# Kernel optimization log

Hardware: AMD Instinct MI355X
Metric: run time of the kernel (lower is better)

The kernel has to match this reference:

```python
import jax, jax.numpy as jnp
import numpy as np

D_MODEL, D_STATE, EXPAND = 1024, 128, 2
E = D_MODEL * EXPAND          # 2048
N = D_STATE                   # 128
H = 1
P = E
TD = D_STATE // 2             # 64
Z_DIM = E + E + N + N + H + H + TD + H  # 4369
EPS = 1e-05
B_SZ, L = 4, 2048


def setup_inputs() -> dict:
    key = jax.random.key(0)
    ks = jax.random.split(key, 6)
    u = jax.random.normal(ks[0], (B_SZ, L, D_MODEL), dtype=jnp.float32)
    W_in = jax.random.normal(ks[1], (Z_DIM, D_MODEL), dtype=jnp.float32) * 0.02
    W_out = jax.random.normal(ks[2], (D_MODEL, E), dtype=jnp.float32) * 0.02
    w_normB = jnp.ones((N,), jnp.float32)
    w_normC = jnp.ones((N,), jnp.float32)
    B_bias = jnp.ones((N,), jnp.float32)
    C_bias = jnp.ones((N,), jnp.float32)
    # dt_bias buffer: dt_i ~ logU(0.001, 0.1); dt_bias = dt_i + log(-expm1(-dt_i))
    dt_i = jnp.exp(jax.random.uniform(ks[3], (H,)) * (np.log(0.1) - np.log(0.001)) + np.log(0.001))
    dt_i = jnp.clip(dt_i, 1e-4, None)
    dt_bias = dt_i + jnp.log(-jnp.expm1(-dt_i))
    A_log = jnp.full((H,), np.log(0.5), jnp.float32)
    return {"u": u, "W_in": W_in, "w_normB": w_normB, "w_normC": w_normC,
            "B_bias": B_bias, "C_bias": C_bias, "dt_bias": dt_bias,
            "A_log": A_log, "W_out": W_out}


def _rms(x, w):
    return x * jax.lax.rsqrt(jnp.mean(x * x, axis=-1, keepdims=True) + EPS) * w


def _rope(x, ang):
    half = x.shape[-1] // 2
    x1, x2 = x[..., :half], x[..., half:]
    c, s = jnp.cos(ang), jnp.sin(ang)
    return jnp.concatenate([x1 * c - x2 * s, x1 * s + x2 * c], axis=-1)


def reference(u, W_in, w_normB, w_normC, B_bias, C_bias, dt_bias, A_log, W_out):
    Bb, Ls, _ = u.shape
    z = u @ W_in.T  # [B, L, Z_DIM]
    o = 0
    def take(n):
        nonlocal o
        r = z[..., o:o + n]; o += n; return r
    x = jax.nn.silu(take(E))
    gate = jax.nn.silu(take(E))
    B_ = take(N)
    C_ = take(N)
    dt_ = take(H)
    A_ = take(H)
    th = take(TD)
    lam_ = take(H)

    dt = jax.nn.softplus(dt_ + dt_bias)          # [B, L, H]
    A = -jax.nn.softplus(A_ + A_log)             # [B, L, H]
    lam = jax.nn.sigmoid(lam_)                   # [B, L, H]
    alpha = jnp.exp(dt * A)                      # [B, L, H]

    B_ = _rms(B_, w_normB) + B_bias
    C_ = _rms(C_, w_normC) + C_bias
    ca = jnp.cumsum(jnp.mean(dt, axis=-1, keepdims=True) * th, axis=1)  # [B, L, TD]
    B_ = _rope(B_, ca)
    C_ = _rope(C_, ca)

    xh = x.reshape(Bb, Ls, H, P)
    xp = jnp.concatenate([jnp.zeros_like(xh[:, :1]), xh[:, :-1]], axis=1)  # roll + zero t=0
    lh = lam[..., None]
    xt = lh * xh + (1.0 - lh) * alpha[..., None] * xp  # [B, L, H, P]

    # fallback SSM: per-channel mean drive, per-head scalar A (mean over batch+time)
    u_mean = jnp.mean(xt, axis=-1)               # [B, L, H]
    A_bar = jnp.mean(A, axis=(0, 1))             # [H]
    dA = jnp.exp(dt * A_bar)                     # [B, L, H]
    dBu = dt[..., None] * B_[:, :, None, :] * u_mean[..., None]  # [B, L, H, N]

    def step(state, xs):
        dA_t, dBu_t, C_t = xs                    # [B,H], [B,H,N], [B,N]
        state = dA_t[..., None] * state + dBu_t  # [B, H, N]
        y_t = jnp.einsum('bhn,bn->bh', state, C_t)
        return state, y_t

    state0 = jnp.zeros((Bb, H, N), dtype=xt.dtype)
    _, ys = jax.lax.scan(step, state0,
                         (jnp.moveaxis(dA, 1, 0), jnp.moveaxis(dBu, 1, 0), jnp.moveaxis(C_, 1, 0)))
    outs = jnp.moveaxis(ys, 0, 1)                # [B, L, H]
    y = jnp.broadcast_to(outs, (Bb, Ls, E))      # H=1 expanded to E
    return (y * gate) @ W_out.T
```

## Files before the change

### kernel.cpp

```cpp
#include <hip/hip_runtime.h>
#include <cstdint>
#include <cstddef>

typedef __bf16 bf16_t;
typedef bf16_t bf16x8 __attribute__((ext_vector_type(8)));
typedef float f32x4 __attribute__((ext_vector_type(4)));

#define B_SZ    4
#define LSEQ    2048
#define DMODEL  1024
#define EDIM    2048
#define ZDIM    4419
#define ZPAD    4608
#define ROWS    (B_SZ*LSEQ)
#define EPSV    1e-5f

#define SCHUNK  128
#define SCLEN   (LSEQ/SCHUNK)
#define RCH     128
#define RCLEN   (LSEQ/RCH)

__device__ __forceinline__ float softplus_f(float x){
  return fmaxf(x, 0.f) + log1pf(expf(-fabsf(x)));
}
__device__ __forceinline__ float sigmoid_f(float x){ return 1.f/(1.f+expf(-x)); }
__device__ __forceinline__ float silu_f(float x){ return x/(1.f+expf(-x)); }

__device__ __forceinline__ void gload_lds16(const void* g, void* l){
  __builtin_amdgcn_global_load_lds(
      (const __attribute__((address_space(1))) void*)g,
      (__attribute__((address_space(3))) void*)l, 16, 0, 0);
}

__device__ __forceinline__ float blockReduce128(float v, float* red, int t){
  red[t] = v; __syncthreads();
  #pragma unroll
  for (int off = 64; off > 0; off >>= 1){
    if (t < off) red[t] += red[t+off];
    __syncthreads();
  }
  float r = red[0];
  __syncthreads();
  return r;
}

__global__ __launch_bounds__(256) void prep_kernel(
    const float* __restrict__ u, const float* __restrict__ win, const float* __restrict__ wout,
    bf16_t* __restrict__ ubf, bf16_t* __restrict__ winbf, bf16_t* __restrict__ woutbf,
    float* __restrict__ Asum, float* __restrict__ xraw)
{
  size_t i = (size_t)blockIdx.x*256 + threadIdx.x;
  if (i == 0) Asum[0] = 0.f;
  if (i < ROWS) xraw[i] = 0.f;
  const size_t NU = (size_t)ROWS*DMODEL;
  const size_t NW = (size_t)ZPAD*DMODEL;
  const size_t NO = (size_t)DMODEL*EDIM;
  if (i < NU){ ubf[i] = (bf16_t)u[i]; return; }
  i -= NU;
  if (i < NW){
    size_t n = i >> 10;
    winbf[i] = (n < (size_t)ZDIM) ? (bf16_t)win[i] : (bf16_t)0.f;
    return;
  }
  i -= NW;
  if (i < NO) woutbf[i] = (bf16_t)wout[i];
}

template<int BM, int KDIM, int NXT, int MODE>
__global__ __launch_bounds__(512, 2) void gemmDP_kernel(
    const bf16_t* __restrict__ A, const bf16_t* __restrict__ W,
    float* __restrict__ xraw, bf16_t* __restrict__ o_g, float* __restrict__ o_z,
    const float* __restrict__ scale, float* __restrict__ o_f)
{
  constexpr int BN = 256;
  constexpr int NT = KDIM/64;
  constexpr int MR = BM/32;
  constexpr int BUFE = (BM+BN)*64;
  __shared__ __align__(16) bf16_t lds[BUFE*3];

  const int tid = threadIdx.x;
  const int wid = tid>>6, lane = tid&63;
  const int wr = wid>>2, wc = wid&3;
  const int lr = lane&15;

  const int nwg = NXT*(ROWS/BM);
  const int id = blockIdx.x;
  const int rid = (id & 7)*(nwg>>3) + (id>>3);
  const int bx = rid % NXT, by = rid / NXT;
  const int m0 = by*BM, n0 = bx*BN;

  f32x4 acc[MR][4] = {};

  auto stage = [&](int buf, int t){
    bf16_t* lA = lds + buf*BUFE;
    bf16_t* lB = lA + BM*64;
    const int k0 = t*64;
    #pragma unroll
    for (int q = 0; q < BM/64; ++q){
      int cidx = q*512 + tid;
      int row = cidx>>3, sc = (cidx&7) ^ (row&7);
      gload_lds16(A + (size_t)(m0+row)*KDIM + k0 + sc*8,
                  lA + (size_t)(q*512 + wid*64)*8);
    }
    #pragma unroll
    for (int q = 0; q < BN/64; ++q){
      int cidx = q*512 + tid;
      int row = cidx>>3, sc = (cidx&7) ^ (row&7);
      gload_lds16(W + (size_t)(n0+row)*KDIM + k0 + sc*8,
                  lB + (size_t)(q*512 + wid*64)*8);
    }
  };

  auto compute = [&](int buf){
    const bf16_t* lA = lds + buf*BUFE;
    const bf16_t* lB = lA + BM*64;
    #pragma unroll
    for (int kk = 0; kk < 2; ++kk){
      const int g = kk*4 + (lane>>4);
      bf16x8 bfr[4], af[MR];
      #pragma unroll
      for (int n = 0; n < 4; ++n){
        int rr = wc*64 + n*16 + lr;
        bfr[n] = *(const bf16x8*)&lB[rr*64 + ((g^(rr&7))<<3)];
      }
      #pragma unroll
      for (int m = 0; m < MR; ++m){
        int rr = wr*(BM/2) + m*16 + lr;
        af[m] = *(const bf16x8*)&lA[rr*64 + ((g^(rr&7))<<3)];
      }
      __builtin_amdgcn_s_setprio(1);
      #pragma unroll
      for (int m = 0; m < MR; ++m)
        #pragma unroll
        for (int n = 0; n < 4; ++n)
          acc[m][n] = __builtin_amdgcn_mfma_f32_16x16x32_bf16(af[m], bfr[n], acc[m][n], 0,0,0);
      __builtin_amdgcn_s_setprio(0);
    }
  };

  stage(0, 0);
  stage(1, 1);
  int cur = 0;
  for (int t = 0; t + 2 < NT; ++t){
    int nb = cur + 2; if (nb >= 3) nb -= 3;
    stage(nb, t+2);
    asm volatile("s_waitcnt vmcnt(12)" ::: "memory");
    asm volatile("s_barrier" ::: "memory");
    compute(cur);
    asm volatile("s_barrier" ::: "memory");
    if (++cur == 3) cur = 0;
  }
  asm volatile("s_waitcnt vmcnt(6)" ::: "memory");
  asm volatile("s_barrier" ::: "memory");
  compute(cur);
  asm volatile("s_barrier" ::: "memory");
  if (++cur == 3) cur = 0;
  asm volatile("s_waitcnt vmcnt(0)" ::: "memory");
  asm volatile("s_barrier" ::: "memory");
  compute(cur);

  if (MODE == 0 && n0 < 2048){
    #pragma unroll
    for (int m = 0; m < MR; ++m){
      #pragma unroll
      for (int i = 0; i < 4; ++i){
        float p = 0.f;
        #pragma unroll
        for (int n = 0; n < 4; ++n) p += silu_f(acc[m][n][i]);
        #pragma unroll
        for (int off = 8; off > 0; off >>= 1) p += __shfl_xor(p, off);
        if (lr == 0){
          int r = m0 + wr*(BM/2) + m*16 + ((lane>>4)<<2) + i;
          atomicAdd(xraw + r, p);
        }
      }
    }
  } else {
    #pragma unroll
    for (int m = 0; m < MR; ++m){
      int rowb = m0 + wr*(BM/2) + m*16 + ((lane>>4)<<2);
      #pragma unroll
      for (int n = 0; n < 4; ++n){
        int col = n0 + wc*64 + n*16 + lr;
        #pragma unroll
        for (int i = 0; i < 4; ++i){
          int r = rowb + i;
          float v = acc[m][n][i];
          if (MODE == 0){
            if (col < 4096)      o_g[(size_t)r*EDIM + (col-2048)] = (bf16_t)silu_f(v);
            else if (col < 4480) o_z[(size_t)r*384 + (col-4096)]  = v;
          } else {
            o_f[(size_t)r*DMODEL + col] = v * scale[r];
          }
        }
      }
    }
  }
}

__global__ __launch_bounds__(128) void fuse_kernel(
    const float* __restrict__ xraw, const float* __restrict__ zs,
    const float* __restrict__ wnB, const float* __restrict__ wnC,
    const float* __restrict__ Bb, const float* __restrict__ Cb,
    const float* __restrict__ dtb, const float* __restrict__ Alog,
    float* __restrict__ Bn, float* __restrict__ Cn, float* __restrict__ dtth,
    float* __restrict__ dts, float* __restrict__ alphas, float* __restrict__ lams,
    float* __restrict__ xbar, float* Asum)
{
  __shared__ float red[128];
  int r = blockIdx.x, t = threadIdx.x;
  const float* zr = zs + (size_t)r*384;
  float bv = zr[t], cv = zr[128+t];
  float b2 = blockReduce128(bv*bv, red, t);
  float c2 = blockReduce128(cv*cv, red, t);
  float rb = rsqrtf(b2*(1.f/128.f) + EPSV);
  float rc = rsqrtf(c2*(1.f/128.f) + EPSV);
  Bn[(size_t)r*128 + t] = bv*rb*wnB[t] + Bb[t];
  Cn[(size_t)r*128 + t] = cv*rc*wnC[t] + Cb[t];

  float dt = softplus_f(zr[256] + dtb[0]);
  if (t < 64) dtth[(size_t)r*64 + t] = dt * zr[258+t];
  if (t == 0){
    float Av  = -softplus_f(zr[257] + Alog[0]);
    float lam = sigmoid_f(zr[322]);
    dts[r]    = dt;
    alphas[r] = expf(dt*Av);
    lams[r]   = lam;
    xbar[r]   = xraw[r] * (1.f/2048.f);
    atomicAdd(Asum, Av);
  }
}

__global__ __launch_bounds__(64) void rope_sum_kernel(
    const float* __restrict__ dtth, float* __restrict__ csum)
{
  int b  = blockIdx.x >> 7;
  int ch = blockIdx.x & 127;
  int d  = threadIdx.x;
  const float* base = dtth + ((size_t)b*LSEQ + (size_t)ch*RCLEN)*64 + d;
  float s = 0.f;
  #pragma unroll
  for (int i = 0; i < RCLEN; ++i) s += base[(size_t)i*64];
  csum[((size_t)b*RCH + ch)*64 + d] = s;
}

__global__ __launch_bounds__(64) void rope_prefix_kernel(float* __restrict__ csum)
{
  int b = blockIdx.x, d = threadIdx.x;
  float s = 0.f;
  for (int c = 0; c < RCH; ++c){
    size_t idx = ((size_t)b*RCH + c)*64 + d;
    float v = csum[idx]; csum[idx] = s; s += v;
  }
}

__global__ __launch_bounds__(64) void rope_apply_kernel(
    const float* __restrict__ dtth, const float* __restrict__ csum,
    float* __restrict__ Bn, float* __restrict__ Cn)
{
  int b  = blockIdx.x >> 7;
  int ch = blockIdx.x & 127;
  int d  = threadIdx.x;
  float ca = csum[((size_t)b*RCH + ch)*64 + d];
  int l0 = ch*RCLEN;
  const float* base = dtth + ((size_t)b*LSEQ)*64 + d;
  for (int l = l0; l < l0 + RCLEN; ++l){
    ca += base[(size_t)l*64];
    float sn, cs;
    sincosf(ca, &sn, &cs);
    size_t ro = ((size_t)b*LSEQ + l)*128;
    float b1 = Bn[ro+d], b2v = Bn[ro+64+d];
    Bn[ro+d]    = b1*cs - b2v*sn;
    Bn[ro+64+d] = b1*sn + b2v*cs;
    float c1 = Cn[ro+d], c2v = Cn[ro+64+d];
    Cn[ro+d]    = c1*cs - c2v*sn;
    Cn[ro+64+d] = c1*sn + c2v*cs;
  }
}

__global__ __launch_bounds__(64) void scan_local_kernel(
    const float* __restrict__ dts, const float* __restrict__ alphas,
    const float* __restrict__ lams, const float* __restrict__ xbar,
    const float* __restrict__ Asum,
    const float* __restrict__ Bn, const float* __restrict__ Cn,
    float* __restrict__ ylocal, float* __restrict__ Pfix,
    float* __restrict__ Sfin, float* __restrict__ Dch)
{
  int b  = blockIdx.x / SCHUNK;
  int ch = blockIdx.x % SCHUNK;
  int n  = threadIdx.x;
  float Abar = Asum[0] * (1.f/(float)ROWS);
  float s1 = 0.f, s2 = 0.f, P = 1.f;
  int l0 = ch*SCLEN;
  #pragma unroll
  for (int i = 0; i < SCLEN; ++i){
    int l = l0 + i;
    size_t r = (size_t)b*LSEQ + l;
    float dt = dts[r], lam = lams[r], al = alphas[r], xb = xbar[r];
    float xp = (l > 0) ? xbar[r-1] : 0.f;
    float um = lam*xb + (1.f-lam)*al*xp;
    float dA = expf(dt*Abar);
    float coef = dt*um;
    size_t ro = r*128;
    s1 = dA*s1 + coef*Bn[ro+n];
    s2 = dA*s2 + coef*Bn[ro+64+n];
    P *= dA;
    float p = s1*Cn[ro+n] + s2*Cn[ro+64+n];
    #pragma unroll
    for (int off = 32; off > 0; off >>= 1) p += __shfl_down(p, off);
    if (n == 0){ ylocal[r] = p; Pfix[r] = P; }
  }
  size_t so = ((size_t)b*SCHUNK + ch)*128;
  Sfin[so + n]      = s1;
  Sfin[so + 64 + n] = s2;
  if (n == 0) Dch[b*SCHUNK + ch] = P;
}

__global__ __launch_bounds__(128) void scan_carry_kernel(
    const float* __restrict__ Sfin, const float* __restrict__ Dch,
    float* __restrict__ Sin)
{
  int b = blockIdx.x;
  int n = threadIdx.x;
  float s = 0.f;
  for (int c = 0; c < SCHUNK; ++c){
    size_t so = ((size_t)b*SCHUNK + c)*128;
    Sin[so + n] = s;
    s = Dch[b*SCHUNK + c]*s + Sfin[so + n];
  }
}

__global__ __launch_bounds__(256) void scan_fix_kernel(
    const float* __restrict__ Cn, const float* __restrict__ Sin,
    const float* __restrict__ ylocal, const float* __restrict__ Pfix,
    float* __restrict__ outsv)
{
  int r = blockIdx.x*4 + (threadIdx.x>>6);
  int n = threadIdx.x & 63;
  int b  = r / LSEQ;
  int ch = (r % LSEQ) / SCLEN;
  const float* si = Sin + ((size_t)b*SCHUNK + ch)*128;
  size_t ro = (size_t)r*128;
  float p = Cn[ro+n]*si[n] + Cn[ro+64+n]*si[64+n];
  #pragma unroll
  for (int off = 32; off > 0; off >>= 1) p += __shfl_down(p, off);
  if (n == 0) outsv[r] = ylocal[r] + Pfix[r]*p;
}

extern "C" void kernel_launch(void* const* d_in, const int* in_sizes, int n_in,
                              void* d_out, int out_size, void* d_ws, size_t ws_size,
                              hipStream_t stream)
{
  const float* u    = (const float*)d_in[0];
  const float* W_in = (const float*)d_in[1];
  const float* wnB  = (const float*)d_in[2];
  const float* wnC  = (const float*)d_in[3];
  const float* Bb   = (const float*)d_in[4];
  const float* Cb   = (const float*)d_in[5];
  const float* dtb  = (const float*)d_in[6];
  const float* Alog = (const float*)d_in[7];
  const float* Wout = (const float*)d_in[8];
  float* out = (float*)d_out;
  char* ws = (char*)d_ws;

  constexpr size_t OFF_ASUM = 0;
  constexpr size_t OFF_UBF  = 256;
  constexpr size_t SZ_UBF   = (size_t)ROWS*DMODEL*2;
  constexpr size_t OFF_WIN  = OFF_UBF + SZ_UBF;
  constexpr size_t SZ_WIN   = (size_t)ZPAD*DMODEL*2;
  constexpr size_t OFF_WOUT = OFF_WIN + SZ_WIN;
  constexpr size_t SZ_WOUT  = (size_t)DMODEL*EDIM*2;
  constexpr size_t OFF_X    = OFF_WOUT + SZ_WOUT;
  constexpr size_t SZ_X     = (size_t)ROWS*EDIM*2;
  constexpr size_t OFF_G    = OFF_X + SZ_X;
  constexpr size_t OFF_ZS   = OFF_G + SZ_X;
  constexpr size_t SZ_ZS    = (size_t)ROWS*384*4;
  constexpr size_t OFF_BN   = OFF_ZS + SZ_ZS;
  constexpr size_t SZ_BN    = (size_t)ROWS*128*4;
  constexpr size_t OFF_CN   = OFF_BN + SZ_BN;
  constexpr size_t OFF_DTTH = OFF_CN + SZ_BN;
  constexpr size_t SZ_DTTH  = (size_t)ROWS*64*4;
  constexpr size_t OFF_DT   = OFF_DTTH + SZ_DTTH;
  constexpr size_t OFF_AL   = OFF_DT  + (size_t)ROWS*4;
  constexpr size_t OFF_LAM  = OFF_AL  + (size_t)ROWS*4;
  constexpr size_t OFF_XB   = OFF_LAM + (size_t)ROWS*4;
  constexpr size_t OFF_OUTS = OFF_XB  + (size_t)ROWS*4;
  constexpr size_t OFF_YLOC = OFF_OUTS + (size_t)ROWS*4;
  constexpr size_t OFF_PFIX = OFF_YLOC + (size_t)ROWS*4;
  constexpr size_t OFF_SFIN = OFF_PFIX + (size_t)ROWS*4;
  constexpr size_t SZ_SFIN  = (size_t)B_SZ*SCHUNK*128*4;
  constexpr size_t OFF_DCH  = OFF_SFIN + SZ_SFIN;
  constexpr size_t OFF_SIN  = OFF_DCH + (size_t)B_SZ*SCHUNK*4;
  constexpr size_t OFF_CSUM = OFF_SIN + SZ_SFIN;

  float*  Asum   = (float*) (ws + OFF_ASUM);
  bf16_t* ubf    = (bf16_t*)(ws + OFF_UBF);
  bf16_t* winbf  = (bf16_t*)(ws + OFF_WIN);
  bf16_t* woutbf = (bf16_t*)(ws + OFF_WOUT);
  float*  xraw   = (float*) (ws + OFF_X);
  bf16_t* gbuf   = (bf16_t*)(ws + OFF_G);
  float*  zsb    = (float*) (ws + OFF_ZS);
  float*  Bn     = (float*) (ws + OFF_BN);
  float*  Cn     = (float*) (ws + OFF_CN);
  float*  dtth   = (float*) (ws + OFF_DTTH);
  float*  dts    = (float*) (ws + OFF_DT);
  float*  alphas = (float*) (ws + OFF_AL);
  float*  lams   = (float*) (ws + OFF_LAM);
  float*  xbar   = (float*) (ws + OFF_XB);
  float*  outsv  = (float*) (ws + OFF_OUTS);
  float*  ylocal = (float*) (ws + OFF_YLOC);
  float*  Pfix   = (float*) (ws + OFF_PFIX);
  float*  Sfin   = (float*) (ws + OFF_SFIN);
  float*  Dch    = (float*) (ws + OFF_DCH);
  float*  Sin    = (float*) (ws + OFF_SIN);
  float*  csum   = (float*) (ws + OFF_CSUM);

  {
    size_t total = (size_t)ROWS*DMODEL + (size_t)ZPAD*DMODEL + (size_t)DMODEL*EDIM;
    int blocks = (int)((total + 255)/256);
    prep_kernel<<<blocks, 256, 0, stream>>>(u, W_in, Wout, ubf, winbf, woutbf, Asum, xraw);
  }
  gemmDP_kernel<128, DMODEL, ZPAD/256, 0><<<(ZPAD/256)*(ROWS/128), 512, 0, stream>>>(
      ubf, winbf, xraw, gbuf, zsb, nullptr, nullptr);
  fuse_kernel<<<ROWS, 128, 0, stream>>>(xraw, zsb, wnB, wnC, Bb, Cb, dtb, Alog,
                                        Bn, Cn, dtth, dts, alphas, lams, xbar, Asum);
  rope_sum_kernel<<<B_SZ*RCH, 64, 0, stream>>>(dtth, csum);
  rope_prefix_kernel<<<B_SZ, 64, 0, stream>>>(csum);
  rope_apply_kernel<<<B_SZ*RCH, 64, 0, stream>>>(dtth, csum, Bn, Cn);
  scan_local_kernel<<<B_SZ*SCHUNK, 64, 0, stream>>>(dts, alphas, lams, xbar, Asum,
                                                    Bn, Cn, ylocal, Pfix, Sfin, Dch);
  scan_carry_kernel<<<B_SZ, 128, 0, stream>>>(Sfin, Dch, Sin);
  scan_fix_kernel<<<ROWS/4, 256, 0, stream>>>(Cn, Sin, ylocal, Pfix, outsv);
  gemmDP_kernel<128, EDIM, DMODEL/256, 1><<<(DMODEL/256)*(ROWS/128), 512, 0, stream>>>(
      gbuf, woutbf, nullptr, nullptr, nullptr, outsv, out);
}
```

Measured before the change: 338.0 us.

## Pad GEMM operand row strides and split staging across two k-substeps

Operands of both GEMMs are now stored with padded leading dimensions (1088 for u/W_in, 2112 for gate/W_out). The aim is to avoid the channel and bank aliasing caused by power-of-two row strides. The main loop is also restructured: A and B tile loads are issued separately, with the B load interleaved between the two k-substeps, and explicit lgkmcnt waits and sched barriers are added to overlap global loads with MFMA work. The padding enlarges the workspace and the prep kernel writes become strided. The extra barrier per iteration could add synchronization cost.

```diff
diff --git a/kernel.cpp b/kernel.cpp
--- a/kernel.cpp
+++ b/kernel.cpp
@@ -15,6 +15,9 @@
 #define ROWS    (B_SZ*LSEQ)
 #define EPSV    1e-5f
 
+#define LDU     1088
+#define LDG     2112
+
 #define SCHUNK  128
 #define SCLEN   (LSEQ/SCHUNK)
 #define RCH     128
@@ -55,25 +58,32 @@
   const size_t NU = (size_t)ROWS*DMODEL;
   const size_t NW = (size_t)ZPAD*DMODEL;
   const size_t NO = (size_t)DMODEL*EDIM;
-  if (i < NU){ ubf[i] = (bf16_t)u[i]; return; }
+  if (i < NU){
+    size_t row = i >> 10, col = i & 1023;
+    ubf[row*LDU + col] = (bf16_t)u[i];
+    return;
+  }
   i -= NU;
   if (i < NW){
-    size_t n = i >> 10;
-    winbf[i] = (n < (size_t)ZDIM) ? (bf16_t)win[i] : (bf16_t)0.f;
+    size_t row = i >> 10, col = i & 1023;
+    winbf[row*LDU + col] = (row < (size_t)ZDIM) ? (bf16_t)win[i] : (bf16_t)0.f;
     return;
   }
   i -= NW;
-  if (i < NO) woutbf[i] = (bf16_t)wout[i];
-}
-
-template<int BM, int KDIM, int NXT, int MODE>
-__global__ __launch_bounds__(512, 2) void gemmDP_kernel(
-    const bf16_t* __restrict__ A, const bf16_t* __restrict__ W,
+  if (i < NO){
+    size_t row = i >> 11, col = i & 2047;
+    woutbf[row*LDG + col] = (bf16_t)wout[i];
+  }
+}
+
+template<int BM, int NT, int NXT, int MODE>
+__global__ __launch_bounds__(512, 2) void gemmP_kernel(
+    const bf16_t* __restrict__ A, const int lda,
+    const bf16_t* __restrict__ W, const int ldw,
     float* __restrict__ xraw, bf16_t* __restrict__ o_g, float* __restrict__ o_z,
     const float* __restrict__ scale, float* __restrict__ o_f)
 {
   constexpr int BN = 256;
-  constexpr int NT = KDIM/64;
   constexpr int MR = BM/32;
   constexpr int BUFE = (BM+BN)*64;
   __shared__ __align__(16) bf16_t lds[BUFE*3];
@@ -91,73 +101,85 @@
 
   f32x4 acc[MR][4] = {};
 
-  auto stage = [&](int buf, int t){
+  auto stageA = [&](int buf, int t){
     bf16_t* lA = lds + buf*BUFE;
-    bf16_t* lB = lA + BM*64;
     const int k0 = t*64;
     #pragma unroll
     for (int q = 0; q < BM/64; ++q){
       int cidx = q*512 + tid;
       int row = cidx>>3, sc = (cidx&7) ^ (row&7);
-      gload_lds16(A + (size_t)(m0+row)*KDIM + k0 + sc*8,
+      gload_lds16(A + (size_t)(m0+row)*lda + k0 + sc*8,
                   lA + (size_t)(q*512 + wid*64)*8);
     }
-    #pragma unroll
-    for (int q = 0; q < BN/64; ++q){
+  };
+  auto stageB = [&](int buf, int t){
+    bf16_t* lB = lds + buf*BUFE + BM*64;
+    const int k0 = t*64;
+    #pragma unroll
+    for (int q = 0; q < 4; ++q){
       int cidx = q*512 + tid;
       int row = cidx>>3, sc = (cidx&7) ^ (row&7);
-      gload_lds16(W + (size_t)(n0+row)*KDIM + k0 + sc*8,
+      gload_lds16(W + (size_t)(n0+row)*ldw + k0 + sc*8,
                   lB + (size_t)(q*512 + wid*64)*8);
     }
   };
-
-  auto compute = [&](int buf){
+  auto dsread = [&](int buf, int kk, bf16x8* af, bf16x8* bfr){
     const bf16_t* lA = lds + buf*BUFE;
     const bf16_t* lB = lA + BM*64;
-    #pragma unroll
-    for (int kk = 0; kk < 2; ++kk){
-      const int g = kk*4 + (lane>>4);
-      bf16x8 bfr[4], af[MR];
+    const int g = kk*4 + (lane>>4);
+    #pragma unroll
+    for (int n = 0; n < 4; ++n){
+      int rr = wc*64 + n*16 + lr;
+      bfr[n] = *(const bf16x8*)&lB[rr*64 + ((g^(rr&7))<<3)];
+    }
+    #pragma unroll
+    for (int m = 0; m < MR; ++m){
+      int rr = wr*(BM/2) + m*16 + lr;
+      af[m] = *(const bf16x8*)&lA[rr*64 + ((g^(rr&7))<<3)];
+    }
+  };
+  auto domfma = [&](bf16x8* af, bf16x8* bfr){
+    asm volatile("s_waitcnt lgkmcnt(0)" ::: "memory");
+    __builtin_amdgcn_sched_barrier(0);
+    __builtin_amdgcn_s_setprio(1);
+    #pragma unroll
+    for (int m = 0; m < MR; ++m)
       #pragma unroll
-      for (int n = 0; n < 4; ++n){
-        int rr = wc*64 + n*16 + lr;
-        bfr[n] = *(const bf16x8*)&lB[rr*64 + ((g^(rr&7))<<3)];
-      }
-      #pragma unroll
-      for (int m = 0; m < MR; ++m){
-        int rr = wr*(BM/2) + m*16 + lr;
-        af[m] = *(const bf16x8*)&lA[rr*64 + ((g^(rr&7))<<3)];
-      }
-      __builtin_amdgcn_s_setprio(1);
-      #pragma unroll
-      for (int m = 0; m < MR; ++m)
-        #pragma unroll
-        for (int n = 0; n < 4; ++n)
-          acc[m][n] = __builtin_amdgcn_mfma_f32_16x16x32_bf16(af[m], bfr[n], acc[m][n], 0,0,0);
-      __builtin_amdgcn_s_setprio(0);
-    }
+      for (int n = 0; n < 4; ++n)
+        acc[m][n] = __builtin_amdgcn_mfma_f32_16x16x32_bf16(af[m], bfr[n], acc[m][n], 0,0,0);
+    __builtin_amdgcn_s_setprio(0);
   };
 
-  stage(0, 0);
-  stage(1, 1);
+  stageA(0,0); stageB(0,0);
+  stageA(1,1); stageB(1,1);
   int cur = 0;
-  for (int t = 0; t + 2 < NT; ++t){
-    int nb = cur + 2; if (nb >= 3) nb -= 3;
-    stage(nb, t+2);
-    asm volatile("s_waitcnt vmcnt(12)" ::: "memory");
+  for (int t = 0; t < NT; ++t){
+    int nb = cur+2; if (nb >= 3) nb -= 3;
+    const bool st = (t+2 < NT);
+    if (st){
+      stageA(nb, t+2);
+      asm volatile("s_waitcnt vmcnt(8)" ::: "memory");
+    } else if (t+1 < NT){
+      asm volatile("s_waitcnt vmcnt(6)" ::: "memory");
+    } else {
+      asm volatile("s_waitcnt vmcnt(0)" ::: "memory");
+    }
     asm volatile("s_barrier" ::: "memory");
-    compute(cur);
+    {
+      bf16x8 af[MR], bfr[4];
+      dsread(cur, 0, af, bfr);
+      domfma(af, bfr);
+    }
+    asm volatile("s_barrier" ::: "memory");
+    {
+      bf16x8 af[MR], bfr[4];
+      dsread(cur, 1, af, bfr);
+      if (st) stageB(nb, t+2);
+      domfma(af, bfr);
+    }
     asm volatile("s_barrier" ::: "memory");
     if (++cur == 3) cur = 0;
   }
-  asm volatile("s_waitcnt vmcnt(6)" ::: "memory");
-  asm volatile("s_barrier" ::: "memory");
-  compute(cur);
-  asm volatile("s_barrier" ::: "memory");
-  if (++cur == 3) cur = 0;
-  asm volatile("s_waitcnt vmcnt(0)" ::: "memory");
-  asm volatile("s_barrier" ::: "memory");
-  compute(cur);
 
   if (MODE == 0 && n0 < 2048){
     #pragma unroll
@@ -187,8 +209,8 @@
           int r = rowb + i;
           float v = acc[m][n][i];
           if (MODE == 0){
-            if (col < 4096)      o_g[(size_t)r*EDIM + (col-2048)] = (bf16_t)silu_f(v);
-            else if (col < 4480) o_z[(size_t)r*384 + (col-4096)]  = v;
+            if (col < 4096)      o_g[(size_t)r*LDG + (col-2048)] = (bf16_t)silu_f(v);
+            else if (col < 4480) o_z[(size_t)r*384 + (col-4096)] = v;
           } else {
             o_f[(size_t)r*DMODEL + col] = v * scale[r];
           }
@@ -365,22 +387,22 @@
 
   constexpr size_t OFF_ASUM = 0;
   constexpr size_t OFF_UBF  = 256;
-  constexpr size_t SZ_UBF   = (size_t)ROWS*DMODEL*2;
+  constexpr size_t SZ_UBF   = (size_t)ROWS*LDU*2;
   constexpr size_t OFF_WIN  = OFF_UBF + SZ_UBF;
-  constexpr size_t SZ_WIN   = (size_t)ZPAD*DMODEL*2;
+  constexpr size_t SZ_WIN   = (size_t)ZPAD*LDU*2;
   constexpr size_t OFF_WOUT = OFF_WIN + SZ_WIN;
-  constexpr size_t SZ_WOUT  = (size_t)DMODEL*EDIM*2;
-  constexpr size_t OFF_X    = OFF_WOUT + SZ_WOUT;
-  constexpr size_t SZ_X     = (size_t)ROWS*EDIM*2;
-  constexpr size_t OFF_G    = OFF_X + SZ_X;
-  constexpr size_t OFF_ZS   = OFF_G + SZ_X;
+  constexpr size_t SZ_WOUT  = (size_t)DMODEL*LDG*2;
+  constexpr size_t OFF_G    = OFF_WOUT + SZ_WOUT;
+  constexpr size_t SZ_G     = (size_t)ROWS*LDG*2;
+  constexpr size_t OFF_ZS   = OFF_G + SZ_G;
   constexpr size_t SZ_ZS    = (size_t)ROWS*384*4;
   constexpr size_t OFF_BN   = OFF_ZS + SZ_ZS;
   constexpr size_t SZ_BN    = (size_t)ROWS*128*4;
   constexpr size_t OFF_CN   = OFF_BN + SZ_BN;
   constexpr size_t OFF_DTTH = OFF_CN + SZ_BN;
   constexpr size_t SZ_DTTH  = (size_t)ROWS*64*4;
-  constexpr size_t OFF_DT   = OFF_DTTH + SZ_DTTH;
+  constexpr size_t OFF_XRAW = OFF_DTTH + SZ_DTTH;
+  constexpr size_t OFF_DT   = OFF_XRAW + (size_t)ROWS*4;
   constexpr size_t OFF_AL   = OFF_DT  + (size_t)ROWS*4;
   constexpr size_t OFF_LAM  = OFF_AL  + (size_t)ROWS*4;
   constexpr size_t OFF_XB   = OFF_LAM + (size_t)ROWS*4;
@@ -397,12 +419,12 @@
   bf16_t* ubf    = (bf16_t*)(ws + OFF_UBF);
   bf16_t* winbf  = (bf16_t*)(ws + OFF_WIN);
   bf16_t* woutbf = (bf16_t*)(ws + OFF_WOUT);
-  float*  xraw   = (float*) (ws + OFF_X);
   bf16_t* gbuf   = (bf16_t*)(ws + OFF_G);
   float*  zsb    = (float*) (ws + OFF_ZS);
   float*  Bn     = (float*) (ws + OFF_BN);
   float*  Cn     = (float*) (ws + OFF_CN);
   float*  dtth   = (float*) (ws + OFF_DTTH);
+  float*  xraw   = (float*) (ws + OFF_XRAW);
   float*  dts    = (float*) (ws + OFF_DT);
   float*  alphas = (float*) (ws + OFF_AL);
   float*  lams   = (float*) (ws + OFF_LAM);
@@ -420,8 +442,8 @@
     int blocks = (int)((total + 255)/256);
     prep_kernel<<<blocks, 256, 0, stream>>>(u, W_in, Wout, ubf, winbf, woutbf, Asum, xraw);
   }
-  gemmDP_kernel<128, DMODEL, ZPAD/256, 0><<<(ZPAD/256)*(ROWS/128), 512, 0, stream>>>(
-      ubf, winbf, xraw, gbuf, zsb, nullptr, nullptr);
+  gemmP_kernel<128, DMODEL/64, ZPAD/256, 0><<<(ZPAD/256)*(ROWS/128), 512, 0, stream>>>(
+      ubf, LDU, winbf, LDU, xraw, gbuf, zsb, nullptr, nullptr);
   fuse_kernel<<<ROWS, 128, 0, stream>>>(xraw, zsb, wnB, wnC, Bb, Cb, dtb, Alog,
                                         Bn, Cn, dtth, dts, alphas, lams, xbar, Asum);
   rope_sum_kernel<<<B_SZ*RCH, 64, 0, stream>>>(dtth, csum);
@@ -431,6 +453,6 @@
                                                     Bn, Cn, ylocal, Pfix, Sfin, Dch);
   scan_carry_kernel<<<B_SZ, 128, 0, stream>>>(Sfin, Dch, Sin);
   scan_fix_kernel<<<ROWS/4, 256, 0, stream>>>(Cn, Sin, ylocal, Pfix, outsv);
-  gemmDP_kernel<128, EDIM, DMODEL/256, 1><<<(DMODEL/256)*(ROWS/128), 512, 0, stream>>>(
-      gbuf, woutbf, nullptr, nullptr, nullptr, outsv, out);
-}
+  gemmP_kernel<128, EDIM/64, DMODEL/256, 1><<<(DMODEL/256)*(ROWS/128), 512, 0, stream>>>(
+      gbuf, LDG, woutbf, LDG, nullptr, nullptr, nullptr, outsv, out);
+}
```

Result: no change. 332.8 us (-1.6%).
